# Optimization experiments

Measured on AMD Instinct MI355X. Metric: run time of the kernel, lower is better.

## Reference

```python
import jax, jax.numpy as jnp
import numpy as np

N = 20000      # nodes
E = 320000     # edges (avg degree 16)
IN = 512       # input feature dim
HID = 64       # hidden_dim
NH = 8         # n_heads
NC = 20        # n_classes
NG = 64        # graphs in batch
EPS = 1e-5     # batchnorm eps


def setup_inputs() -> dict:
    key = jax.random.key(0)
    ks = jax.random.split(key, 32)
    rn = lambda k, shape, s=0.05: (jax.random.normal(k, shape, jnp.float32) * s)
    inp = {
        "x": rn(ks[0], (N, IN), 1.0),
        "src": jax.random.randint(ks[1], (E,), 0, N),
        "dst": jax.random.randint(ks[2], (E,), 0, N),
        "graph_ids": jnp.sort(jax.random.randint(ks[3], (N,), 0, NG)),
        "n_graphs": NG,
        # encoder
        "W_enc": rn(ks[4], (IN, HID)), "b_enc": jnp.zeros((HID,), jnp.float32),
        # GAT layer 0
        "fc_W0": rn(ks[5], (HID, NH * HID)),
        "attn_l0": rn(ks[6], (NH, HID)), "attn_r0": rn(ks[7], (NH, HID)),
        "res_W0": rn(ks[8], (HID, NH * HID)),
        "bias0": jnp.zeros((NH * HID,), jnp.float32),
        "dp_W0": rn(ks[9], (NH * HID, HID)), "dp_b0": jnp.zeros((HID,), jnp.float32),
        # GAT layer 1
        "fc_W1": rn(ks[10], (HID, NH * HID)),
        "attn_l1": rn(ks[11], (NH, HID)), "attn_r1": rn(ks[12], (NH, HID)),
        "res_W1": rn(ks[13], (HID, NH * HID)),
        "bias1": jnp.zeros((NH * HID,), jnp.float32),
        "dp_W1": rn(ks[14], (NH * HID, HID)), "dp_b1": jnp.zeros((HID,), jnp.float32),
        # batchnorm affine
        "gamma": jnp.ones((2 * HID,), jnp.float32), "beta": jnp.zeros((2 * HID,), jnp.float32),
        # global attention pooling gate
        "gate_W": rn(ks[15], (2 * HID, 1)), "gate_b": jnp.zeros((1,), jnp.float32),
        # classifier
        "cls_W": rn(ks[16], (2 * HID, NC)), "cls_b": jnp.zeros((NC,), jnp.float32),
    }
    return inp


def gat_conv(h, fc_W, attn_l, attn_r, res_W, bias, src, dst, n_nodes):
    # DGL GATConv: fc -> per-head scalar scores -> edge softmax over incoming
    # edges -> weighted sum -> residual + bias -> leaky_relu activation.
    nh, d = attn_l.shape
    feat = (h @ fc_W).reshape(n_nodes, nh, d)              # [N,H,D]
    el = jnp.sum(feat * attn_l[None], axis=-1)             # [N,H]
    er = jnp.sum(feat * attn_r[None], axis=-1)             # [N,H]
    e = jax.nn.leaky_relu(el[src] + er[dst], 0.2)          # [E,H]
    m = jax.ops.segment_max(e, dst, num_segments=n_nodes)  # segment softmax
    ex = jnp.exp(e - m[dst])
    denom = jax.ops.segment_sum(ex, dst, num_segments=n_nodes)
    a = ex / denom[dst]                                    # [E,H]
    msg = feat[src] * a[:, :, None]                        # [E,H,D]  (dominant)
    rst = jax.ops.segment_sum(msg, dst, num_segments=n_nodes)  # [N,H,D]
    rst = rst + (h @ res_W).reshape(n_nodes, nh, d) + bias.reshape(nh, d)
    return jax.nn.leaky_relu(rst, 0.01)  # F.leaky_relu default slope


def reference(x, W_enc, b_enc,
              fc_W0, attn_l0, attn_r0, res_W0, bias0, dp_W0, dp_b0,
              fc_W1, attn_l1, attn_r1, res_W1, bias1, dp_W1, dp_b1,
              gamma, beta, gate_W, gate_b, cls_W, cls_b,
              src, dst, graph_ids, n_graphs):
    n_nodes = x.shape[0]
    he = x @ W_enc + b_enc                                  # encoder [N,HID]
    h = he
    h = gat_conv(h, fc_W0, attn_l0, attn_r0, res_W0, bias0, src, dst, n_nodes)
    h = h.reshape(n_nodes, -1) @ dp_W0 + dp_b0              # down_proj 0
    h = gat_conv(h, fc_W1, attn_l1, attn_r1, res_W1, bias1, src, dst, n_nodes)
    h = h.reshape(n_nodes, -1) @ dp_W1 + dp_b1              # down_proj 1
    hg = jnp.concatenate([h, he], axis=1)                   # [N,2*HID]
    # BatchNorm1d (training-mode batch stats, biased variance)
    mu = jnp.mean(hg, axis=0)
    var = jnp.var(hg, axis=0)
    hg = (hg - mu) * jax.lax.rsqrt(var + EPS) * gamma + beta
    # GlobalAttentionPooling: per-graph softmax over node gates
    gate = hg @ gate_W + gate_b                             # [N,1]
    gm = jax.ops.segment_max(gate, graph_ids, num_segments=n_graphs)
    ge = jnp.exp(gate - gm[graph_ids])
    gden = jax.ops.segment_sum(ge, graph_ids, num_segments=n_graphs)
    alpha = ge / gden[graph_ids]                            # [N,1]
    readout = jax.ops.segment_sum(alpha * hg, graph_ids, num_segments=n_graphs)
    return readout @ cls_W + cls_b                          # [NG,NC]
```

## Files before the change

kernel.cpp:

```cpp
#include <hip/hip_runtime.h>
#include <hip/hip_bf16.h>

#define MROWS   20000
#define N_EDGES 320000
#define DIN     512
#define HID     64
#define NH      8
#define ND      512
#define NCLS    20
#define NG      64
#define BN_EPS  1e-5f
#define PCH     16
#define BNB     256
#define TPB     128
#define AGG_NBLK  125
#define AGG_CHUNK 160

typedef __hip_bfloat16 bf16;
typedef __attribute__((ext_vector_type(8))) short s16x8;
typedef __attribute__((ext_vector_type(4))) short s16x4;
typedef __attribute__((ext_vector_type(4))) float f32x4;
typedef __attribute__((ext_vector_type(4))) unsigned int u32x4;
typedef __attribute__((ext_vector_type(2))) float f32x2;

enum { TF32 = 0, TBF16 = 1, TMODE = 2 };

__device__ __forceinline__ int is_bf16_mode(const void* gamma) {
    return *(const unsigned*)gamma != 0x3F800000u;
}

__device__ __forceinline__ float ld_f32(const void* p, size_t i) { return ((const float*)p)[i]; }
__device__ __forceinline__ float ld_b16(const void* p, size_t i) { return __bfloat162float(((const bf16*)p)[i]); }

template<int T>
__device__ __forceinline__ float ldT(const void* p, size_t i, int bf) {
    if constexpr (T == TF32) return ld_f32(p, i);
    else if constexpr (T == TBF16) return ld_b16(p, i);
    else return bf ? ld_b16(p, i) : ld_f32(p, i);
}
template<int T>
__device__ __forceinline__ void stT(void* p, size_t i, int bf, float v) {
    if constexpr (T == TF32) ((float*)p)[i] = v;
    else if constexpr (T == TBF16) ((bf16*)p)[i] = __float2bfloat16(v);
    else { if (bf) ((bf16*)p)[i] = __float2bfloat16(v); else ((float*)p)[i] = v; }
}

__device__ __forceinline__ float bfbits2f(short s) {
    return __uint_as_float(((unsigned)(unsigned short)s) << 16);
}
__device__ __forceinline__ short f2bfbits(float v) {
    bf16 b = __float2bfloat16(v);
    return *reinterpret_cast<short*>(&b);
}

struct TP { const void* src[7]; bf16* dst[7]; int K[7]; };
__global__ void prep_kernel(TP tp, const void* __restrict__ gamma, int* __restrict__ zero0) {
    int b = blockIdx.x;
    int z = b * 256 + threadIdx.x;
    if (z < 2 * MROWS) zero0[z] = 0;
    const int bf = is_bf16_mode(gamma);
    int id = b / TPB;
    int i = (b - id * TPB) * 256 + threadIdx.x;
    int K = tp.K[id];
    int N = (DIN * HID) / K;
    int n = i / K, k = i - n * K;
    tp.dst[id][i] = __float2bfloat16(ldT<TMODE>(tp.src[id], (size_t)k * N + n, bf));
}

__global__ void hist_kernel(const int* __restrict__ keys, int* __restrict__ counts, int n) {
    int i = blockIdx.x * 256 + threadIdx.x;
    if (i < n) atomicAdd(&counts[keys[i]], 1);
}

__global__ __launch_bounds__(1024)
void scan_all_kernel(const int* __restrict__ counts, int* __restrict__ offs,
                     const int* __restrict__ gids, int* __restrict__ goffs) {
    if (threadIdx.x <= NG) {
        int g = threadIdx.x;
        int lo = 0, hi = MROWS;
        while (lo < hi) {
            int mid = (lo + hi) >> 1;
            if (gids[mid] < g) lo = mid + 1; else hi = mid;
        }
        goffs[g] = lo;
    }
    __shared__ int wsum[16];
    __shared__ int carry_s;
    int carry = 0;
    int lane = threadIdx.x & 63, wid = threadIdx.x >> 6;
    const int NCHUNK = (MROWS + 1023) / 1024;
    for (int ch = 0; ch < NCHUNK; ++ch) {
        int i = ch * 1024 + threadIdx.x;
        int v = (i < MROWS) ? counts[i] : 0;
        int s = v;
        #pragma unroll
        for (int o = 1; o < 64; o <<= 1) { int t = __shfl_up(s, o, 64); if (lane >= o) s += t; }
        if (lane == 63) wsum[wid] = s;
        __syncthreads();
        if (wid == 0 && lane < 16) {
            int t = wsum[lane];
            #pragma unroll
            for (int o = 1; o < 16; o <<= 1) { int u = __shfl_up(t, o, 64); if (lane >= o) t += u; }
            wsum[lane] = t;
        }
        __syncthreads();
        int wc = (wid > 0) ? wsum[wid - 1] : 0;
        int incl = s + wc + carry;
        if (i < MROWS) offs[i] = incl - v;
        if (threadIdx.x == 1023) carry_s = incl;
        __syncthreads();
        carry = carry_s;
    }
    if (threadIdx.x == 0) offs[MROWS] = carry;
}

__global__ void scatter_kernel(const int* __restrict__ src, const int* __restrict__ dst,
                               const int* __restrict__ offs, int* __restrict__ cursor,
                               int* __restrict__ src_sorted) {
    int e = blockIdx.x * 256 + threadIdx.x;
    if (e < N_EDGES) {
        int d = dst[e];
        int pos = offs[d] + atomicAdd(&cursor[d], 1);
        src_sorted[pos] = src[e];
    }
}

template<int K, int NB, int NTOT, bool XF32>
__global__ __launch_bounds__(256)
void gemm_mfma(const void* __restrict__ Araw, const bf16* __restrict__ BT,
               const void* __restrict__ bias, bf16* __restrict__ C,
               const void* __restrict__ gamma) {
    const int bf = is_bf16_mode(gamma);
    const int wid  = threadIdx.x >> 6;
    const int lane = threadIdx.x & 63;
    const int quad = lane >> 4;
    const int l16  = lane & 15;
    const int rb = blockIdx.x * 128 + wid * 32;
    const int cb = blockIdx.y * NB;
    constexpr int CT = NB / 16;
    constexpr int KC = K / 32;

    f32x4 acc[2][CT] = {};
    int r0 = rb + l16;       if (r0 >= MROWS) r0 = MROWS - 1;
    int r1 = rb + 16 + l16;  if (r1 >= MROWS) r1 = MROWS - 1;

    auto lda = [&](int row, int koff) -> s16x8 {
        if (XF32 && !bf) {
            const float* fp = (const float*)Araw + (size_t)row * K + koff;
            float4 u = *(const float4*)fp;
            float4 v = *(const float4*)(fp + 4);
            s16x8 r;
            r[0] = f2bfbits(u.x); r[1] = f2bfbits(u.y); r[2] = f2bfbits(u.z); r[3] = f2bfbits(u.w);
            r[4] = f2bfbits(v.x); r[5] = f2bfbits(v.y); r[6] = f2bfbits(v.z); r[7] = f2bfbits(v.w);
            return r;
        }
        return *(const s16x8*)((const bf16*)Araw + (size_t)row * K + koff);
    };
    const bf16* btp = BT + (size_t)(cb + l16) * K + quad * 8;

    for (int kc = 0; kc < KC; ++kc) {
        s16x8 af0 = lda(r0, quad * 8 + kc * 32);
        s16x8 af1 = lda(r1, quad * 8 + kc * 32);
        s16x8 bfr[CT];
        #pragma unroll
        for (int ct = 0; ct < CT; ++ct)
            bfr[ct] = *(const s16x8*)(btp + (size_t)ct * 16 * K + kc * 32);
        #pragma unroll
        for (int ct = 0; ct < CT; ++ct) {
            acc[0][ct] = __builtin_amdgcn_mfma_f32_16x16x32_bf16(bfr[ct], af0, acc[0][ct], 0, 0, 0);
            acc[1][ct] = __builtin_amdgcn_mfma_f32_16x16x32_bf16(bfr[ct], af1, acc[1][ct], 0, 0, 0);
        }
    }
    #pragma unroll
    for (int ct = 0; ct < CT; ++ct) {
        int c0 = cb + ct * 16 + quad * 4;
        float b0 = bias ? ldT<TMODE>(bias, c0 + 0, bf) : 0.f;
        float b1 = bias ? ldT<TMODE>(bias, c0 + 1, bf) : 0.f;
        float b2 = bias ? ldT<TMODE>(bias, c0 + 2, bf) : 0.f;
        float b3 = bias ? ldT<TMODE>(bias, c0 + 3, bf) : 0.f;
        #pragma unroll
        for (int rt = 0; rt < 2; ++rt) {
            int row = rb + rt * 16 + l16;
            if (row < MROWS) {
                s16x4 o;
                o[0] = f2bfbits(acc[rt][ct][0] + b0);
                o[1] = f2bfbits(acc[rt][ct][1] + b1);
                o[2] = f2bfbits(acc[rt][ct][2] + b2);
                o[3] = f2bfbits(acc[rt][ct][3] + b3);
                *(s16x4*)(C + (size_t)row * NTOT + c0) = o;
            }
        }
    }
}

__global__ __launch_bounds__(256)
void gemm_fcres(const bf16* __restrict__ A, const bf16* __restrict__ BT_fc,
                const bf16* __restrict__ BT_res, const void* __restrict__ bias,
                bf16* __restrict__ feat, bf16* __restrict__ rst,
                const void* __restrict__ gamma) {
    const int bf = is_bf16_mode(gamma);
    const bool isres = blockIdx.y >= 4;
    const int yy = blockIdx.y & 3;
    const bf16* BT = isres ? BT_res : BT_fc;
    bf16* C = isres ? rst : feat;
    const int wid  = threadIdx.x >> 6;
    const int lane = threadIdx.x & 63;
    const int quad = lane >> 4;
    const int l16  = lane & 15;
    const int rb = blockIdx.x * 128 + wid * 32;
    const int cb = yy * 128;
    constexpr int CT = 8;
    constexpr int K  = HID;
    constexpr int KC = K / 32;

    f32x4 acc[2][CT] = {};
    int r0 = rb + l16;       if (r0 >= MROWS) r0 = MROWS - 1;
    int r1 = rb + 16 + l16;  if (r1 >= MROWS) r1 = MROWS - 1;
    const bf16* a0p = A + (size_t)r0 * K + quad * 8;
    const bf16* a1p = A + (size_t)r1 * K + quad * 8;
    const bf16* btp = BT + (size_t)(cb + l16) * K + quad * 8;

    #pragma unroll
    for (int kc = 0; kc < KC; ++kc) {
        s16x8 af0 = *(const s16x8*)(a0p + kc * 32);
        s16x8 af1 = *(const s16x8*)(a1p + kc * 32);
        s16x8 bfr[CT];
        #pragma unroll
        for (int ct = 0; ct < CT; ++ct)
            bfr[ct] = *(const s16x8*)(btp + (size_t)ct * 16 * K + kc * 32);
        #pragma unroll
        for (int ct = 0; ct < CT; ++ct) {
            acc[0][ct] = __builtin_amdgcn_mfma_f32_16x16x32_bf16(bfr[ct], af0, acc[0][ct], 0, 0, 0);
            acc[1][ct] = __builtin_amdgcn_mfma_f32_16x16x32_bf16(bfr[ct], af1, acc[1][ct], 0, 0, 0);
        }
    }
    #pragma unroll
    for (int ct = 0; ct < CT; ++ct) {
        int c0 = cb + ct * 16 + quad * 4;
        float b0 = isres ? ldT<TMODE>(bias, c0 + 0, bf) : 0.f;
        float b1 = isres ? ldT<TMODE>(bias, c0 + 1, bf) : 0.f;
        float b2 = isres ? ldT<TMODE>(bias, c0 + 2, bf) : 0.f;
        float b3 = isres ? ldT<TMODE>(bias, c0 + 3, bf) : 0.f;
        #pragma unroll
        for (int rt = 0; rt < 2; ++rt) {
            int row = rb + rt * 16 + l16;
            if (row < MROWS) {
                s16x4 o;
                o[0] = f2bfbits(acc[rt][ct][0] + b0);
                o[1] = f2bfbits(acc[rt][ct][1] + b1);
                o[2] = f2bfbits(acc[rt][ct][2] + b2);
                o[3] = f2bfbits(acc[rt][ct][3] + b3);
                *(s16x4*)(C + (size_t)row * ND + c0) = o;
            }
        }
    }
}

__global__ __launch_bounds__(256)
void elr_kernel(const bf16* __restrict__ feat, const void* __restrict__ attn_l,
                const void* __restrict__ attn_r, float* __restrict__ el,
                float* __restrict__ er, const void* __restrict__ gamma) {
    const int bf = is_bf16_mode(gamma);
    const int b = blockIdx.x;
    const int hx = b & 7;
    const int chunk = b >> 3;
    const int g = threadIdx.x >> 3;
    const int l8 = threadIdx.x & 7;
    const int base = hx * 64 + l8 * 8;
    float al[8], ar[8];
    #pragma unroll
    for (int j = 0; j < 8; ++j) {
        al[j] = ldT<TMODE>(attn_l, base + j, bf);
        ar[j] = ldT<TMODE>(attn_r, base + j, bf);
    }
    for (int n = chunk * AGG_CHUNK + g; n < (chunk + 1) * AGG_CHUNK; n += 32) {
        s16x8 f = *(const s16x8*)(feat + (size_t)n * ND + base);
        float e = 0.f, r = 0.f;
        #pragma unroll
        for (int j = 0; j < 8; ++j) {
            float v = bfbits2f(f[j]);
            e += v * al[j];
            r += v * ar[j];
        }
        e += __shfl_xor(e, 1, 64); e += __shfl_xor(e, 2, 64); e += __shfl_xor(e, 4, 64);
        r += __shfl_xor(r, 1, 64); r += __shfl_xor(r, 2, 64); r += __shfl_xor(r, 4, 64);
        if (l8 == 0) el[n * 8 + hx] = e;
        if (l8 == 1) er[n * 8 + hx] = r;
    }
}

__global__ __launch_bounds__(256)
void agg_kernel(const bf16* __restrict__ feat, const float* __restrict__ el,
                const float* __restrict__ er, const int* __restrict__ offs,
                const int* __restrict__ srcs, bf16* __restrict__ rst) {
    const int b = blockIdx.x;
    const int hx = b & 7;
    const int chunk = b >> 3;
    const int g = threadIdx.x >> 3;
    const int l8 = threadIdx.x & 7;
    const int base = hx * 64 + l8 * 8;

    for (int n = chunk * AGG_CHUNK + g; n < (chunk + 1) * AGG_CHUNK; n += 32) {
        int e0 = offs[n], e1 = offs[n + 1];
        float er_h = er[n * 8 + hx];
        f32x2 acc2[4] = {};
        float den = 0.f;
        for (int eb = e0; eb < e1; eb += 4) {
            int last = e1 - 1;
            int i1 = eb + 1 > last ? last : eb + 1;
            int i2 = eb + 2 > last ? last : eb + 2;
            int i3 = eb + 3 > last ? last : eb + 3;
            int s0 = srcs[eb], s1 = srcs[i1], s2 = srcs[i2], s3 = srcs[i3];
            float l0 = el[s0 * 8 + hx], l1 = el[s1 * 8 + hx];
            float l2 = el[s2 * 8 + hx], l3 = el[s3 * 8 + hx];
            u32x4 f0 = *(const u32x4*)(feat + (size_t)s0 * ND + base);
            u32x4 f1 = *(const u32x4*)(feat + (size_t)s1 * ND + base);
            u32x4 f2 = *(const u32x4*)(feat + (size_t)s2 * ND + base);
            u32x4 f3 = *(const u32x4*)(feat + (size_t)s3 * ND + base);
            float sc0 = l0 + er_h; sc0 = sc0 > 0.f ? sc0 : 0.2f * sc0;
            float sc1 = l1 + er_h; sc1 = sc1 > 0.f ? sc1 : 0.2f * sc1;
            float sc2 = l2 + er_h; sc2 = sc2 > 0.f ? sc2 : 0.2f * sc2;
            float sc3 = l3 + er_h; sc3 = sc3 > 0.f ? sc3 : 0.2f * sc3;
            float w0 = __expf(fminf(sc0, 30.f));
            float w1 = __expf(fminf(sc1, 30.f));
            float w2 = __expf(fminf(sc2, 30.f));
            float w3 = __expf(fminf(sc3, 30.f));
            int rem = e1 - eb;
            if (rem < 4) {
                if (rem < 2) w1 = 0.f;
                if (rem < 3) w2 = 0.f;
                w3 = 0.f;
            }
            den += w0 + w1 + w2 + w3;
            f32x2 w20 = {w0, w0}, w21 = {w1, w1}, w22 = {w2, w2}, w23 = {w3, w3};
            #pragma unroll
            for (int q = 0; q < 4; ++q) {
                f32x2 x0, x1, x2, x3;
                x0[0] = __uint_as_float(f0[q] << 16); x0[1] = __uint_as_float(f0[q] & 0xffff0000u);
                x1[0] = __uint_as_float(f1[q] << 16); x1[1] = __uint_as_float(f1[q] & 0xffff0000u);
                x2[0] = __uint_as_float(f2[q] << 16); x2[1] = __uint_as_float(f2[q] & 0xffff0000u);
                x3[0] = __uint_as_float(f3[q] << 16); x3[1] = __uint_as_float(f3[q] & 0xffff0000u);
                acc2[q] += x0 * w20;
                acc2[q] += x1 * w21;
                acc2[q] += x2 * w22;
                acc2[q] += x3 * w23;
            }
        }
        float inv = (den > 0.f) ? 1.f / den : 0.f;
        s16x8* rp = (s16x8*)(rst + (size_t)n * ND + base);
        s16x8 rr = *rp;
        s16x8 ro;
        #pragma unroll
        for (int q = 0; q < 4; ++q) {
            float rlo = bfbits2f(rr[2 * q])     + acc2[q][0] * inv;
            float rhi = bfbits2f(rr[2 * q + 1]) + acc2[q][1] * inv;
            rlo = rlo > 0.f ? rlo : 0.01f * rlo;
            rhi = rhi > 0.f ? rhi : 0.01f * rhi;
            ro[2 * q]     = f2bfbits(rlo);
            ro[2 * q + 1] = f2bfbits(rhi);
        }
        *rp = ro;
    }
}

__global__ void bn_part_kernel(const bf16* __restrict__ h2, const bf16* __restrict__ he,
                               float* __restrict__ psum, float* __restrict__ psq) {
    int t = threadIdx.x;
    int b = blockIdx.x;
    int beg = (int)((long)MROWS * b / BNB);
    int end = (int)((long)MROWS * (b + 1) / BNB);
    const bf16* srcb = (t < 64) ? h2 : he;
    int col = t & 63;
    float s = 0.f, s2 = 0.f;
    for (int r = beg; r < end; ++r) {
        float v = __bfloat162float(srcb[(size_t)r * 64 + col]);
        s += v;
        s2 += v * v;
    }
    psum[b * 128 + t] = s;
    psq[b * 128 + t] = s2;
}

__global__ void bn_reduce_kernel(const float* __restrict__ psum, const float* __restrict__ psq,
                                 const void* __restrict__ gamma, const void* __restrict__ beta,
                                 float* __restrict__ scale, float* __restrict__ shift) {
    const int bf = is_bf16_mode(gamma);
    int t = threadIdx.x;
    float s = 0.f, s2 = 0.f;
    for (int b = 0; b < BNB; ++b) { s += psum[b * 128 + t]; s2 += psq[b * 128 + t]; }
    float mu = s * (1.f / MROWS);
    float var = s2 * (1.f / MROWS) - mu * mu;
    float inv = rsqrtf(fmaxf(var, 0.f) + BN_EPS);
    float a = ldT<TMODE>(gamma, t, bf) * inv;
    scale[t] = a;
    shift[t] = ldT<TMODE>(beta, t, bf) - mu * a;
}

__global__ __launch_bounds__(128)
void poolgate_kernel(const bf16* __restrict__ h2, const bf16* __restrict__ he,
                     const float* __restrict__ scale, const float* __restrict__ shift,
                     const void* __restrict__ gate_W, const void* __restrict__ gate_b,
                     const int* __restrict__ goffs,
                     float* __restrict__ pacc, float* __restrict__ pden,
                     const void* __restrict__ gamma) {
    const int bf = is_bf16_mode(gamma);
    int g = blockIdx.x;
    int c = blockIdx.y;
    int t = threadIdx.x;
    int r0 = goffs[g], r1 = goffs[g + 1];
    int len = r1 - r0;
    int beg = r0 + (int)((long)len * c / PCH);
    int end = r0 + (int)((long)len * (c + 1) / PCH);
    const bf16* srcb = (t < 64) ? h2 : he;
    int col = t & 63;
    float sc = scale[t], sh = shift[t];
    float gw = ldT<TMODE>(gate_W, t, bf);
    float gb = ldT<TMODE>(gate_b, 0, bf);
    __shared__ float ws[2];
    float acc = 0.f, den = 0.f;
    for (int r = beg; r < end; ++r) {
        float v = __bfloat162float(srcb[(size_t)r * 64 + col]) * sc + sh;
        float p = v * gw;
        #pragma unroll
        for (int o = 32; o > 0; o >>= 1) p += __shfl_xor(p, o, 64);
        if ((t & 63) == 0) ws[t >> 6] = p;
        __syncthreads();
        float wg = __expf(fminf(fmaxf(ws[0] + ws[1] + gb, -60.f), 30.f));
        den += wg;
        acc += wg * v;
        __syncthreads();
    }
    pacc[((size_t)g * PCH + c) * 128 + t] = acc;
    if (t == 0) pden[g * PCH + c] = den;
}

__global__ __launch_bounds__(128)
void poolcls_kernel(const float* __restrict__ pacc, const float* __restrict__ pden,
                    const void* __restrict__ W, const void* __restrict__ b,
                    void* __restrict__ out, const void* __restrict__ gamma) {
    const int bf = is_bf16_mode(gamma);
    int g = blockIdx.x;
    int t = threadIdx.x;
    float acc = 0.f, den = 0.f;
    #pragma unroll
    for (int c = 0; c < PCH; ++c) {
        acc += pacc[((size_t)g * PCH + c) * 128 + t];
        den += pden[g * PCH + c];
    }
    __shared__ float rs[128];
    rs[t] = (den > 0.f) ? acc / den : 0.f;
    __syncthreads();
    if (t < NCLS) {
        float o = ldT<TMODE>(b, t, bf);
        #pragma unroll 8
        for (int k = 0; k < 128; ++k)
            o += rs[k] * ldT<TMODE>(W, (size_t)k * NCLS + t, bf);
        stT<TMODE>(out, g * NCLS + t, bf, o);
    }
}

extern "C" void kernel_launch(void* const* d_in, const int* in_sizes, int n_in,
                              void* d_out, int out_size, void* d_ws, size_t ws_size,
                              hipStream_t stream) {
    const void* x       = d_in[0];
    const int*  src     = (const int*)d_in[1];
    const int*  dst     = (const int*)d_in[2];
    const int*  gids    = (const int*)d_in[3];
    const void* W_enc   = d_in[5];
    const void* b_enc   = d_in[6];
    const void* fc_W0   = d_in[7];
    const void* attn_l0 = d_in[8];
    const void* attn_r0 = d_in[9];
    const void* res_W0  = d_in[10];
    const void* bias0   = d_in[11];
    const void* dp_W0   = d_in[12];
    const void* dp_b0   = d_in[13];
    const void* fc_W1   = d_in[14];
    const void* attn_l1 = d_in[15];
    const void* attn_r1 = d_in[16];
    const void* res_W1  = d_in[17];
    const void* bias1   = d_in[18];
    const void* dp_W1   = d_in[19];
    const void* dp_b1   = d_in[20];
    const void* gamma   = d_in[21];
    const void* beta    = d_in[22];
    const void* gate_W  = d_in[23];
    const void* gate_b  = d_in[24];
    const void* cls_W   = d_in[25];
    const void* cls_b   = d_in[26];

    char* wsc = (char*)d_ws;
    size_t off = 0;
    auto alloc = [&](size_t bytes) -> void* {
        void* p = wsc + off;
        off = (off + bytes + 255) & ~(size_t)255;
        return p;
    };
    bf16*  he        = (bf16*) alloc((size_t)MROWS * HID * 2);
    bf16*  h         = (bf16*) alloc((size_t)MROWS * HID * 2);
    bf16*  h2        = (bf16*) alloc((size_t)MROWS * HID * 2);
    bf16*  feat      = (bf16*) alloc((size_t)MROWS * ND * 2);
    bf16*  rst       = (bf16*) alloc((size_t)MROWS * ND * 2);
    bf16*  bt_enc    = (bf16*) alloc((size_t)DIN * HID * 2);
    bf16*  bt_fc0    = (bf16*) alloc((size_t)HID * ND * 2);
    bf16*  bt_res0   = (bf16*) alloc((size_t)HID * ND * 2);
    bf16*  bt_dp0    = (bf16*) alloc((size_t)ND * HID * 2);
    bf16*  bt_fc1    = (bf16*) alloc((size_t)HID * ND * 2);
    bf16*  bt_res1   = (bf16*) alloc((size_t)HID * ND * 2);
    bf16*  bt_dp1    = (bf16*) alloc((size_t)ND * HID * 2);
    float* el        = (float*)alloc((size_t)MROWS * 8 * 4);
    float* er        = (float*)alloc((size_t)MROWS * 8 * 4);
    int*   src_sorted= (int*)  alloc((size_t)N_EDGES * 4);
    int*   offs      = (int*)  alloc((size_t)(MROWS + 1) * 4);
    int*   goffs     = (int*)  alloc((size_t)(NG + 1) * 4);
    float* psum      = (float*)alloc((size_t)BNB * 128 * 4);
    float* psq       = (float*)alloc((size_t)BNB * 128 * 4);
    float* pacc      = (float*)alloc((size_t)NG * PCH * 128 * 4);
    float* pden      = (float*)alloc((size_t)NG * PCH * 4);
    float* bnscale   = (float*)alloc(128 * 4);
    float* bnshift   = (float*)alloc(128 * 4);
    char*  zbase     = (char*) alloc((size_t)MROWS * 4 * 2);
    int* counts  = (int*)zbase;
    int* cursor  = counts + MROWS;

    TP tp;
    tp.src[0] = W_enc;  tp.K[0] = DIN;
    tp.src[1] = fc_W0;  tp.K[1] = HID;
    tp.src[2] = res_W0; tp.K[2] = HID;
    tp.src[3] = dp_W0;  tp.K[3] = ND;
    tp.src[4] = fc_W1;  tp.K[4] = HID;
    tp.src[5] = res_W1; tp.K[5] = HID;
    tp.src[6] = dp_W1;  tp.K[6] = ND;
    tp.dst[0] = bt_enc; tp.dst[1] = bt_fc0; tp.dst[2] = bt_res0; tp.dst[3] = bt_dp0;
    tp.dst[4] = bt_fc1; tp.dst[5] = bt_res1; tp.dst[6] = bt_dp1;
    prep_kernel<<<7 * TPB, 256, 0, stream>>>(tp, gamma, (int*)zbase);

    hist_kernel<<<(N_EDGES + 255) / 256, 256, 0, stream>>>(dst, counts, N_EDGES);
    scan_all_kernel<<<1, 1024, 0, stream>>>(counts, offs, gids, goffs);
    scatter_kernel<<<(N_EDGES + 255) / 256, 256, 0, stream>>>(src, dst, offs, cursor, src_sorted);

    const int GX = (MROWS + 127) / 128;

    gemm_mfma<DIN, 64, 64, true><<<dim3(GX, 1), 256, 0, stream>>>(x, bt_enc, b_enc, he, gamma);

    gemm_fcres<<<dim3(GX, 8), 256, 0, stream>>>(he, bt_fc0, bt_res0, bias0, feat, rst, gamma);
    elr_kernel<<<AGG_NBLK * 8, 256, 0, stream>>>(feat, attn_l0, attn_r0, el, er, gamma);
    agg_kernel<<<AGG_NBLK * 8, 256, 0, stream>>>(feat, el, er, offs, src_sorted, rst);
    gemm_mfma<ND, 64, 64, false><<<dim3(GX, 1), 256, 0, stream>>>(rst, bt_dp0, dp_b0, h, gamma);

    gemm_fcres<<<dim3(GX, 8), 256, 0, stream>>>(h, bt_fc1, bt_res1, bias1, feat, rst, gamma);
    elr_kernel<<<AGG_NBLK * 8, 256, 0, stream>>>(feat, attn_l1, attn_r1, el, er, gamma);
    agg_kernel<<<AGG_NBLK * 8, 256, 0, stream>>>(feat, el, er, offs, src_sorted, rst);
    gemm_mfma<ND, 64, 64, false><<<dim3(GX, 1), 256, 0, stream>>>(rst, bt_dp1, dp_b1, h2, gamma);

    bn_part_kernel<<<BNB, 128, 0, stream>>>(h2, he, psum, psq);
    bn_reduce_kernel<<<1, 128, 0, stream>>>(psum, psq, gamma, beta, bnscale, bnshift);
    poolgate_kernel<<<dim3(NG, PCH), 128, 0, stream>>>(h2, he, bnscale, bnshift, gate_W, gate_b,
                                                       goffs, pacc, pden, gamma);
    poolcls_kernel<<<NG, 128, 0, stream>>>(pacc, pden, cls_W, cls_b, d_out, gamma);
}
```

Before: 464.2 us.

## Precompute per-edge attention exponentials in a separate kernel before aggregation

Adds a wexp_kernel that, for each destination-sorted edge, computes leaky_relu(el[src]+er[dst]) and its exponential for all 8 heads and stores them in a new wpre buffer. The aggregation kernel then reads these precomputed weights instead of gathering el per source and computing exp inline. The scatter step now also records the sorted dst per edge. This takes the scattered el gathers and exp math out of the latency-bound gather loop, at the cost of an extra launch per layer and about 10 MB of write plus read traffic per layer.

Measured after the change: 472.4 us. Within noise of the previous version (+1.8%).

```diff
diff --git a/kernel.cpp b/kernel.cpp
--- a/kernel.cpp
+++ b/kernel.cpp
@@ -116,12 +116,13 @@
 
 __global__ void scatter_kernel(const int* __restrict__ src, const int* __restrict__ dst,
                                const int* __restrict__ offs, int* __restrict__ cursor,
-                               int* __restrict__ src_sorted) {
+                               int* __restrict__ src_sorted, int* __restrict__ dst_sorted) {
     int e = blockIdx.x * 256 + threadIdx.x;
     if (e < N_EDGES) {
         int d = dst[e];
         int pos = offs[d] + atomicAdd(&cursor[d], 1);
         src_sorted[pos] = src[e];
+        dst_sorted[pos] = d;
     }
 }
 
@@ -290,9 +291,34 @@
 }
 
 __global__ __launch_bounds__(256)
-void agg_kernel(const bf16* __restrict__ feat, const float* __restrict__ el,
-                const float* __restrict__ er, const int* __restrict__ offs,
-                const int* __restrict__ srcs, bf16* __restrict__ rst) {
+void wexp_kernel(const int* __restrict__ src_sorted, const int* __restrict__ dst_sorted,
+                 const float* __restrict__ el, const float* __restrict__ er,
+                 float* __restrict__ wpre) {
+    int e = blockIdx.x * 256 + threadIdx.x;
+    if (e >= N_EDGES) return;
+    int s = src_sorted[e], d = dst_sorted[e];
+    f32x4 a0 = *(const f32x4*)(el + s * 8);
+    f32x4 a1 = *(const f32x4*)(el + s * 8 + 4);
+    f32x4 b0 = *(const f32x4*)(er + d * 8);
+    f32x4 b1 = *(const f32x4*)(er + d * 8 + 4);
+    f32x4 o0, o1;
+    #pragma unroll
+    for (int j = 0; j < 4; ++j) {
+        float sc = a0[j] + b0[j];
+        sc = sc > 0.f ? sc : 0.2f * sc;
+        o0[j] = __expf(fminf(sc, 30.f));
+        float sd = a1[j] + b1[j];
+        sd = sd > 0.f ? sd : 0.2f * sd;
+        o1[j] = __expf(fminf(sd, 30.f));
+    }
+    *(f32x4*)(wpre + (size_t)e * 8)     = o0;
+    *(f32x4*)(wpre + (size_t)e * 8 + 4) = o1;
+}
+
+__global__ __launch_bounds__(256)
+void agg_kernel(const bf16* __restrict__ feat, const float* __restrict__ wpre,
+                const int* __restrict__ offs, const int* __restrict__ srcs,
+                bf16* __restrict__ rst) {
     const int b = blockIdx.x;
     const int hx = b & 7;
     const int chunk = b >> 3;
@@ -302,7 +328,6 @@
 
     for (int n = chunk * AGG_CHUNK + g; n < (chunk + 1) * AGG_CHUNK; n += 32) {
         int e0 = offs[n], e1 = offs[n + 1];
-        float er_h = er[n * 8 + hx];
         f32x2 acc2[4] = {};
         float den = 0.f;
         for (int eb = e0; eb < e1; eb += 4) {
@@ -310,21 +335,15 @@
             int i1 = eb + 1 > last ? last : eb + 1;
             int i2 = eb + 2 > last ? last : eb + 2;
             int i3 = eb + 3 > last ? last : eb + 3;
+            float w0 = wpre[(size_t)eb * 8 + hx];
+            float w1 = wpre[(size_t)i1 * 8 + hx];
+            float w2 = wpre[(size_t)i2 * 8 + hx];
+            float w3 = wpre[(size_t)i3 * 8 + hx];
             int s0 = srcs[eb], s1 = srcs[i1], s2 = srcs[i2], s3 = srcs[i3];
-            float l0 = el[s0 * 8 + hx], l1 = el[s1 * 8 + hx];
-            float l2 = el[s2 * 8 + hx], l3 = el[s3 * 8 + hx];
             u32x4 f0 = *(const u32x4*)(feat + (size_t)s0 * ND + base);
             u32x4 f1 = *(const u32x4*)(feat + (size_t)s1 * ND + base);
             u32x4 f2 = *(const u32x4*)(feat + (size_t)s2 * ND + base);
             u32x4 f3 = *(const u32x4*)(feat + (size_t)s3 * ND + base);
-            float sc0 = l0 + er_h; sc0 = sc0 > 0.f ? sc0 : 0.2f * sc0;
-            float sc1 = l1 + er_h; sc1 = sc1 > 0.f ? sc1 : 0.2f * sc1;
-            float sc2 = l2 + er_h; sc2 = sc2 > 0.f ? sc2 : 0.2f * sc2;
-            float sc3 = l3 + er_h; sc3 = sc3 > 0.f ? sc3 : 0.2f * sc3;
-            float w0 = __expf(fminf(sc0, 30.f));
-            float w1 = __expf(fminf(sc1, 30.f));
-            float w2 = __expf(fminf(sc2, 30.f));
-            float w3 = __expf(fminf(sc3, 30.f));
             int rem = e1 - eb;
             if (rem < 4) {
                 if (rem < 2) w1 = 0.f;
@@ -510,7 +529,9 @@
     bf16*  bt_dp1    = (bf16*) alloc((size_t)ND * HID * 2);
     float* el        = (float*)alloc((size_t)MROWS * 8 * 4);
     float* er        = (float*)alloc((size_t)MROWS * 8 * 4);
+    float* wpre      = (float*)alloc((size_t)N_EDGES * 8 * 4);
     int*   src_sorted= (int*)  alloc((size_t)N_EDGES * 4);
+    int*   dst_sorted= (int*)  alloc((size_t)N_EDGES * 4);
     int*   offs      = (int*)  alloc((size_t)(MROWS + 1) * 4);
     int*   goffs     = (int*)  alloc((size_t)(NG + 1) * 4);
     float* psum      = (float*)alloc((size_t)BNB * 128 * 4);
@@ -537,20 +558,24 @@
 
     hist_kernel<<<(N_EDGES + 255) / 256, 256, 0, stream>>>(dst, counts, N_EDGES);
     scan_all_kernel<<<1, 1024, 0, stream>>>(counts, offs, gids, goffs);
-    scatter_kernel<<<(N_EDGES + 255) / 256, 256, 0, stream>>>(src, dst, offs, cursor, src_sorted);
+    scatter_kernel<<<(N_EDGES + 255) / 256, 256, 0, stream>>>(src, dst, offs, cursor,
+                                                              src_sorted, dst_sorted);
 
     const int GX = (MROWS + 127) / 128;
+    const int EB = (N_EDGES + 255) / 256;
 
     gemm_mfma<DIN, 64, 64, true><<<dim3(GX, 1), 256, 0, stream>>>(x, bt_enc, b_enc, he, gamma);
 
     gemm_fcres<<<dim3(GX, 8), 256, 0, stream>>>(he, bt_fc0, bt_res0, bias0, feat, rst, gamma);
     elr_kernel<<<AGG_NBLK * 8, 256, 0, stream>>>(feat, attn_l0, attn_r0, el, er, gamma);
-    agg_kernel<<<AGG_NBLK * 8, 256, 0, stream>>>(feat, el, er, offs, src_sorted, rst);
+    wexp_kernel<<<EB, 256, 0, stream>>>(src_sorted, dst_sorted, el, er, wpre);
+    agg_kernel<<<AGG_NBLK * 8, 256, 0, stream>>>(feat, wpre, offs, src_sorted, rst);
     gemm_mfma<ND, 64, 64, false><<<dim3(GX, 1), 256, 0, stream>>>(rst, bt_dp0, dp_b0, h, gamma);
 
     gemm_fcres<<<dim3(GX, 8), 256, 0, stream>>>(h, bt_fc1, bt_res1, bias1, feat, rst, gamma);
     elr_kernel<<<AGG_NBLK * 8, 256, 0, stream>>>(feat, attn_l1, attn_r1, el, er, gamma);
-    agg_kernel<<<AGG_NBLK * 8, 256, 0, stream>>>(feat, el, er, offs, src_sorted, rst);
+    wexp_kernel<<<EB, 256, 0, stream>>>(src_sorted, dst_sorted, el, er, wpre);
+    agg_kernel<<<AGG_NBLK * 8, 256, 0, stream>>>(feat, wpre, offs, src_sorted, rst);
     gemm_mfma<ND, 64, 64, false><<<dim3(GX, 1), 256, 0, stream>>>(rst, bt_dp1, dp_b1, h2, gamma);
 
     bn_part_kernel<<<BNB, 128, 0, stream>>>(h2, he, psum, psq);
```
